# Performance work log

Hardware: AMD Instinct MI355X
Metric: run time of the kernel (lower is better)

The kernel has to match this reference:

```python
import jax, jax.numpy as jnp
import numpy as np

HIDDEN = 1024

def _cat_linear(x, W, b, cat_ids):
    # x: (B,T,Din), W: (C,Din,Dout), b: (C,Dout)
    return jnp.einsum('bti,bio->bto', x, W[cat_ids]) + b[cat_ids][:, None, :]

def _sinusoidal(timesteps, dim):
    # timesteps: (B,T) int -> (B,T,dim)
    t = timesteps.astype(jnp.float32)
    half = dim // 2
    exponent = -jnp.arange(half, dtype=jnp.float32) * (jnp.log(10000.0) / half)
    freqs = t[..., None] * jnp.exp(exponent)
    return jnp.concatenate([jnp.sin(freqs), jnp.cos(freqs)], axis=-1)

def setup_inputs() -> dict:
    key = jax.random.key(0)
    ks = jax.random.split(key, 8)
    B, T, A, H, C = 64, 64, 64, HIDDEN, 16
    actions = jax.random.normal(ks[0], (B, T, A), dtype=jnp.float32)
    timesteps = jax.random.randint(ks[1], (B,), 0, 1000)
    cat_ids = jax.random.randint(ks[2], (B,), 0, C)
    W1 = 0.02 * jax.random.normal(ks[3], (C, A, H), dtype=jnp.float32)
    b1 = jnp.zeros((C, H), dtype=jnp.float32)
    W2 = 0.02 * jax.random.normal(ks[4], (C, 2 * H, H), dtype=jnp.float32)
    b2 = jnp.zeros((C, H), dtype=jnp.float32)
    W3 = 0.02 * jax.random.normal(ks[5], (C, H, H), dtype=jnp.float32)
    b3 = jnp.zeros((C, H), dtype=jnp.float32)
    return {"actions": actions, "timesteps": timesteps, "cat_ids": cat_ids,
            "W1": W1, "b1": b1, "W2": W2, "b2": b2, "W3": W3, "b3": b3}

def reference(actions, timesteps, cat_ids, W1, b1, W2, b2, W3, b3):
    B, T, _ = actions.shape
    ts = jnp.broadcast_to(timesteps[:, None], (B, T))  # (B,T)
    a_emb = _cat_linear(actions, W1, b1, cat_ids)        # (B,T,H)
    tau = _sinusoidal(ts, HIDDEN).astype(a_emb.dtype)    # (B,T,H)
    x = jnp.concatenate([a_emb, tau], axis=-1)           # (B,T,2H)
    h = _cat_linear(x, W2, b2, cat_ids)
    h = h * jax.nn.sigmoid(h)                            # swish
    return _cat_linear(h, W3, b3, cat_ids)               # (B,T,H)
```

## Files before the change

### kernel.cpp

```cpp
#include <hip/hip_runtime.h>
#include <hip/hip_bf16.h>
#include <math.h>


typedef short bf16x8 __attribute__((ext_vector_type(8)));
typedef float floatx4 __attribute__((ext_vector_type(4)));

__device__ inline short f2bf(float f) {
  union { float f; unsigned u; } v; v.f = f;
  unsigned u = v.u;
  return (short)(((u + 0x7fffu + ((u >> 16) & 1u)) >> 16) & 0xffffu);
}

__device__ inline unsigned pk2(float a, float b) {
  union { float f; unsigned u; } x, y; x.f = a; y.f = b;
  unsigned ua = (x.u + 0x7fffu + ((x.u >> 16) & 1u)) >> 16;
  unsigned ub = (y.u + 0x7fffu + ((y.u >> 16) & 1u)) >> 16;
  return (ua & 0xffffu) | (ub << 16);
}

#if __has_builtin(__builtin_amdgcn_global_load_lds)
__device__ inline void async16(float* lds, const float* g) {
  __builtin_amdgcn_global_load_lds(
      (const __attribute__((address_space(1))) unsigned int*)g,
      (__attribute__((address_space(3))) unsigned int*)lds, 16, 0, 0);
}
#define ASYNC_LDS 1
#else
__device__ inline void async16(float* lds, const float* g) {
  *(floatx4*)lds = *(const floatx4*)g;
}
#define ASYNC_LDS 0
#endif

__device__ inline void stage_tile(float* tilebuf, const float* __restrict__ Wsrc,
                                  int tid) {
  const int wave = tid >> 6;
#if ASYNC_LDS
  #pragma unroll
  for (int i = 0; i < 4; ++i) {
    const int s  = i * 256 + tid;
    const int k  = s >> 5;
    const int p  = s & 31;
    const int cc = (p - 4 * (k >> 3)) & 31;
    const float* g = Wsrc + (size_t)k * 1024 + cc * 4;
    float* l = tilebuf + (size_t)(i * 256 + wave * 64) * 4;
    async16(l, g);
  }
#else
  #pragma unroll
  for (int i = 0; i < 4; ++i) {
    const int s  = i * 256 + tid;
    const int k  = s >> 5;
    const int p  = s & 31;
    const int cc = (p - 4 * (k >> 3)) & 31;
    *(floatx4*)(tilebuf + (size_t)s * 4) =
        *(const floatx4*)(Wsrc + (size_t)k * 1024 + cc * 4);
  }
#endif
}

__device__ inline bf16x8 read_bfrag(const float* __restrict__ tile, int col, int quad) {
  const int cc = col >> 2, c3 = col & 3;
  const int p  = (cc + 4 * quad) & 31;
  const float* base = tile + (size_t)p * 4 + c3 + (size_t)(quad * 8) * 128;
  float f[8];
  #pragma unroll
  for (int j = 0; j < 8; ++j) f[j] = base[(size_t)j * 128];
  union { bf16x8 v; unsigned u[4]; } r;
  #pragma unroll
  for (int j = 0; j < 4; ++j) r.u[j] = pk2(f[2 * j], f[2 * j + 1]);
  return r.v;
}

template<int K, bool A_F32, bool SWISH, bool OUT_BF16>
__global__ __launch_bounds__(256) void gemm_kernel(
    const void* __restrict__ Aall, int lda,
    const float* __restrict__ Wall,
    const float* __restrict__ bias,
    const int* __restrict__ cat_ids,
    void* __restrict__ Out, int ldo)
{
  constexpr int N  = 1024;
  constexpr int KT = K / 32;
  __shared__ float wtile[2][32 * 128];
  __shared__ int s_b[80], s_c[80], s_np;

  const int tid = threadIdx.x;
  if (tid < 80) { s_b[tid] = -1; s_c[tid] = 0; }
  __syncthreads();
  if (tid < 64) {
    const int myc = cat_ids[tid];
    int rank = 0, pst = 0, tot = 0;
    #pragma unroll
    for (int c = 0; c < 16; ++c) {
      unsigned long long m = __ballot(myc == c);
      const int cnt = __popcll(m);
      const int pc  = 2 * ((cnt + 1) >> 1);
      if (c < myc)  pst += pc;
      if (c == myc) rank = __popcll(m & ((1ull << tid) - 1ull));
      tot += pc;
    }
    const int slot = pst + rank;
    s_b[slot] = tid;
    s_c[slot] = myc;
    if (tid == 0) s_np = tot >> 1;
  }
  __syncthreads();

  const int e = blockIdx.y;
  if (e >= s_np) return;
  const int b0v = s_b[2 * e];
  int b1 = s_b[2 * e + 1];
  const int c = s_c[2 * e];
  const bool st1 = (b1 >= 0);
  if (!st1) b1 = b0v;

  const int wave = tid >> 6, lane = tid & 63;
  const int quad = lane >> 4, l16 = lane & 15;
  const int wm = wave >> 1, wn = wave & 1;
  const int ns = blockIdx.x * 128;
  const float* Wc = Wall + (size_t)c * K * N + ns;

  const char* arow[4];
  #pragma unroll
  for (int mt = 0; mt < 4; ++mt) {
    const int pr = wm * 64 + mt * 16 + l16;
    const int batch = (pr < 64) ? b0v : b1;
    const int row = batch * 64 + (pr & 63);
    arow[mt] = (const char*)Aall + (size_t)row * lda * (A_F32 ? 4 : 2);
  }

  floatx4 acc[4][4];
  #pragma unroll
  for (int mt = 0; mt < 4; ++mt)
    #pragma unroll
    for (int nt = 0; nt < 4; ++nt)
      acc[mt][nt] = (floatx4){0.f, 0.f, 0.f, 0.f};

  stage_tile(&wtile[0][0], Wc, tid);
  int buf = 0;
  for (int kt = 0; kt < KT; ++kt) {
    __syncthreads();
    if (kt + 1 < KT)
      stage_tile(&wtile[buf ^ 1][0], Wc + (size_t)(kt + 1) * 32 * 1024, tid);

    const float* tp = &wtile[buf][0];
    const int kk = kt * 32 + quad * 8;

    bf16x8 af[4];
    #pragma unroll
    for (int mt = 0; mt < 4; ++mt) {
      if constexpr (A_F32) {
        const floatx4* p = (const floatx4*)(arow[mt] + (size_t)kk * 4);
        floatx4 x0 = p[0], x1 = p[1];
        union { bf16x8 v; unsigned u[4]; } t;
        t.u[0] = pk2(x0[0], x0[1]); t.u[1] = pk2(x0[2], x0[3]);
        t.u[2] = pk2(x1[0], x1[1]); t.u[3] = pk2(x1[2], x1[3]);
        af[mt] = t.v;
      } else {
        af[mt] = *(const bf16x8*)(arow[mt] + (size_t)kk * 2);
      }
    }

    #pragma unroll
    for (int nt = 0; nt < 4; ++nt) {
      bf16x8 bf = read_bfrag(tp, wn * 64 + nt * 16 + l16, quad);
      #pragma unroll
      for (int mt = 0; mt < 4; ++mt)
        acc[mt][nt] = __builtin_amdgcn_mfma_f32_16x16x32_bf16(af[mt], bf, acc[mt][nt], 0, 0, 0);
    }
    buf ^= 1;
  }

  #pragma unroll
  for (int nt = 0; nt < 4; ++nt) {
    const int col = ns + wn * 64 + nt * 16 + l16;
    const float bv = bias[(size_t)c * N + col];
    #pragma unroll
    for (int mt = 0; mt < 4; ++mt) {
      const int prb = wm * 64 + mt * 16 + quad * 4;
      const int batch = (prb < 64) ? b0v : b1;
      const bool do_store = (prb < 64) || st1;
      #pragma unroll
      for (int r = 0; r < 4; ++r) {
        const int row = batch * 64 + ((prb + r) & 63);
        float v = acc[mt][nt][r] + bv;
        if constexpr (SWISH) v = v / (1.f + __expf(-v));
        if (do_store) {
          if constexpr (OUT_BF16)
            ((short*)Out)[(size_t)row * ldo + col] = f2bf(v);
          else
            ((float*)Out)[(size_t)row * ldo + col] = v;
        }
      }
    }
  }
}

__global__ __launch_bounds__(256) void tau_kernel(const int* __restrict__ ts,
                                                  short* __restrict__ x)
{
  const int b = blockIdx.x;
  const float t = (float)ts[b];
  const int tid = threadIdx.x;
  #pragma unroll
  for (int q = 0; q < 4; ++q) {
    const int i  = q * 256 + tid;
    const int hi = i & 511;
    const float e = __expf(-(float)hi * 0.017988946039015980f);
    const float freq = t * e;
    const float v = (i < 512) ? sinf(freq) : cosf(freq);
    const short sv = f2bf(v);
    short* base = x + (size_t)(b * 64) * 2048 + 1024 + i;
    #pragma unroll 4
    for (int tt = 0; tt < 64; ++tt) base[(size_t)tt * 2048] = sv;
  }
}

extern "C" void kernel_launch(void* const* d_in, const int* in_sizes, int n_in,
                              void* d_out, int out_size, void* d_ws, size_t ws_size,
                              hipStream_t stream) {
  const float* actions   = (const float*)d_in[0];
  const int*   timesteps = (const int*)  d_in[1];
  const int*   cat_ids   = (const int*)  d_in[2];
  const float* W1 = (const float*)d_in[3];
  const float* b1 = (const float*)d_in[4];
  const float* W2 = (const float*)d_in[5];
  const float* b2 = (const float*)d_in[6];
  const float* W3 = (const float*)d_in[7];
  const float* b3 = (const float*)d_in[8];

  short* x = (short*)d_ws;
  short* h = x + (size_t)64 * 64 * 2048;

  dim3 grid(8, 40), blk(256);

  gemm_kernel<64, true, false, true><<<grid, blk, 0, stream>>>(
      (const void*)actions, 64, W1, b1, cat_ids, (void*)x, 2048);

  tau_kernel<<<64, 256, 0, stream>>>(timesteps, x);

  gemm_kernel<2048, false, true, true><<<grid, blk, 0, stream>>>(
      (const void*)x, 2048, W2, b2, cat_ids, (void*)h, 1024);

  gemm_kernel<1024, false, false, false><<<grid, blk, 0, stream>>>(
      (const void*)h, 1024, W3, b3, cat_ids, d_out, 1024);
}
```

Before: 374.2 us.

## Restructure GEMM into per-wave triple-buffered pipeline and fuse tau into first GEMM

Each wave now owns a private three-slab LDS buffer for a 32-column weight strip and computes all 128 rows. It prefetches weights two k-steps ahead with async global-to-LDS loads and double-buffers A fragments in registers. Explicit vmcnt waits replace block-wide __syncthreads, removing barrier stalls and letting loads overlap with MFMA work. The code also uses the hardware v_cvt_pk_bf16_f32 instruction for fp32-to-bf16 packing, adds launch_bounds occupancy 2, and folds the sinusoidal tau write into the first GEMM kernel to save a launch. The risks are higher register pressure and that the hand-written waitcnt accounting may be fragile.

After: 432.3 us. 15.5% more time.

```diff
diff --git a/kernel.cpp b/kernel.cpp
--- a/kernel.cpp
+++ b/kernel.cpp
@@ -1,5 +1,4 @@
 #include <hip/hip_runtime.h>
-#include <hip/hip_bf16.h>
 #include <math.h>
 
 
@@ -12,78 +11,113 @@
   return (short)(((u + 0x7fffu + ((u >> 16) & 1u)) >> 16) & 0xffffu);
 }
 
-__device__ inline unsigned pk2(float a, float b) {
-  union { float f; unsigned u; } x, y; x.f = a; y.f = b;
-  unsigned ua = (x.u + 0x7fffu + ((x.u >> 16) & 1u)) >> 16;
-  unsigned ub = (y.u + 0x7fffu + ((y.u >> 16) & 1u)) >> 16;
-  return (ua & 0xffffu) | (ub << 16);
+__device__ __forceinline__ unsigned cvtpk(float a, float b) {
+  unsigned r;
+  asm("v_cvt_pk_bf16_f32 %0, %1, %2" : "=v"(r) : "v"(a), "v"(b));
+  return r;
 }
 
 #if __has_builtin(__builtin_amdgcn_global_load_lds)
-__device__ inline void async16(float* lds, const float* g) {
+#define ASYNC_LDS 1
+__device__ __forceinline__ void async16(const float* g, float* lds) {
   __builtin_amdgcn_global_load_lds(
       (const __attribute__((address_space(1))) unsigned int*)g,
       (__attribute__((address_space(3))) unsigned int*)lds, 16, 0, 0);
 }
-#define ASYNC_LDS 1
 #else
-__device__ inline void async16(float* lds, const float* g) {
+#define ASYNC_LDS 0
+__device__ __forceinline__ void async16(const float* g, float* lds) {
   *(floatx4*)lds = *(const floatx4*)g;
 }
-#define ASYNC_LDS 0
 #endif
 
-__device__ inline void stage_tile(float* tilebuf, const float* __restrict__ Wsrc,
-                                  int tid) {
-  const int wave = tid >> 6;
-#if ASYNC_LDS
-  #pragma unroll
-  for (int i = 0; i < 4; ++i) {
-    const int s  = i * 256 + tid;
-    const int k  = s >> 5;
-    const int p  = s & 31;
-    const int cc = (p - 4 * (k >> 3)) & 31;
-    const float* g = Wsrc + (size_t)k * 1024 + cc * 4;
-    float* l = tilebuf + (size_t)(i * 256 + wave * 64) * 4;
-    async16(l, g);
-  }
-#else
-  #pragma unroll
-  for (int i = 0; i < 4; ++i) {
-    const int s  = i * 256 + tid;
-    const int k  = s >> 5;
-    const int p  = s & 31;
-    const int cc = (p - 4 * (k >> 3)) & 31;
-    *(floatx4*)(tilebuf + (size_t)s * 4) =
-        *(const floatx4*)(Wsrc + (size_t)k * 1024 + cc * 4);
-  }
-#endif
-}
-
-__device__ inline bf16x8 read_bfrag(const float* __restrict__ tile, int col, int quad) {
-  const int cc = col >> 2, c3 = col & 3;
-  const int p  = (cc + 4 * quad) & 31;
-  const float* base = tile + (size_t)p * 4 + c3 + (size_t)(quad * 8) * 128;
-  float f[8];
-  #pragma unroll
-  for (int j = 0; j < 8; ++j) f[j] = base[(size_t)j * 128];
-  union { bf16x8 v; unsigned u[4]; } r;
-  #pragma unroll
-  for (int j = 0; j < 4; ++j) r.u[j] = pk2(f[2 * j], f[2 * j + 1]);
-  return r.v;
-}
-
-template<int K, bool A_F32, bool SWISH, bool OUT_BF16>
-__global__ __launch_bounds__(256) void gemm_kernel(
+__device__ __forceinline__ void gload16(floatx4& d, const void* p) {
+  asm volatile("global_load_dwordx4 %0, %1, off" : "=v"(d) : "v"(p) : "memory");
+}
+template<int N> __device__ __forceinline__ void vm_wait() {
+  asm volatile("s_waitcnt vmcnt(%0)" :: "n"(N) : "memory");
+}
+__device__ __forceinline__ void lgkm0() {
+  asm volatile("s_waitcnt lgkmcnt(0)" ::: "memory");
+}
+
+#define KBODY(VMX, LOADA, DOSTAGE, AIN, AOUT)                                  \
+  {                                                                            \
+    lgkm0();                                                                   \
+    if (LOADA) {                                                               \
+      _Pragma("unroll")                                                        \
+      for (int mt = 0; mt < 8; ++mt) {                                         \
+        const char* p = arow[mt] + aoff;                                       \
+        if constexpr (A_F32) {                                                 \
+          gload16(AOUT[2 * mt], p); gload16(AOUT[2 * mt + 1], p + 16);         \
+        } else {                                                               \
+          gload16(AOUT[mt], p);                                                \
+        }                                                                      \
+      }                                                                        \
+      aoff += 32 * AB;                                                         \
+    }                                                                          \
+    if (DOSTAGE) {                                                             \
+      _Pragma("unroll")                                                        \
+      for (int i = 0; i < 4; ++i)                                              \
+        async16((const float*)(wbp + goff[i]), bs + i * 256);                  \
+      wbp += 32 * 1024 * 4;                                                    \
+    }                                                                          \
+    vm_wait<VMX>();                                                            \
+    __builtin_amdgcn_sched_barrier(0);                                         \
+    bf16x8 af[8];                                                              \
+    _Pragma("unroll")                                                          \
+    for (int mt = 0; mt < 8; ++mt) {                                           \
+      if constexpr (A_F32) {                                                   \
+        union { bf16x8 v; unsigned u[4]; } t;                                  \
+        floatx4 x0 = AIN[2 * mt], x1 = AIN[2 * mt + 1];                        \
+        t.u[0] = cvtpk(x0[0], x0[1]); t.u[1] = cvtpk(x0[2], x0[3]);            \
+        t.u[2] = cvtpk(x1[0], x1[1]); t.u[3] = cvtpk(x1[2], x1[3]);            \
+        af[mt] = t.v;                                                          \
+      } else {                                                                 \
+        union { floatx4 f; bf16x8 v; } t; t.f = AIN[mt]; af[mt] = t.v;         \
+      }                                                                        \
+    }                                                                          \
+    _Pragma("unroll")                                                          \
+    for (int nt = 0; nt < 2; ++nt) {                                           \
+      const float* fp = bc + quad * 256 + ((nt * 16 + l16) ^ (quad << 3));     \
+      float f[8];                                                              \
+      _Pragma("unroll")                                                        \
+      for (int j = 0; j < 8; ++j) f[j] = fp[j * 32];                           \
+      union { bf16x8 v; unsigned u[4]; } bb;                                   \
+      _Pragma("unroll")                                                        \
+      for (int j = 0; j < 4; ++j) bb.u[j] = cvtpk(f[2 * j], f[2 * j + 1]);     \
+      _Pragma("unroll")                                                        \
+      for (int mt = 0; mt < 8; ++mt)                                           \
+        acc[mt][nt] = __builtin_amdgcn_mfma_f32_16x16x32_bf16(                 \
+            af[mt], bb.v, acc[mt][nt], 0, 0, 0);                               \
+    }                                                                          \
+    { float* t_ = bc; bc = bn; bn = bs; bs = t_; }                             \
+  }
+
+template<int K, bool A_F32, bool SWISH, bool OUT_BF16, bool TAU>
+__global__ __launch_bounds__(256, 2) void gemm_kernel(
     const void* __restrict__ Aall, int lda,
     const float* __restrict__ Wall,
     const float* __restrict__ bias,
     const int* __restrict__ cat_ids,
-    void* __restrict__ Out, int ldo)
+    void* __restrict__ Out, int ldo,
+    const int* __restrict__ ts)
 {
-  constexpr int N  = 1024;
+  constexpr int NCOL = 1024;
   constexpr int KT = K / 32;
-  __shared__ float wtile[2][32 * 128];
+  constexpr int AB = A_F32 ? 4 : 2;
+  constexpr int AOPS = A_F32 ? 16 : 8;
+#if ASYNC_LDS
+  constexpr int VM_MAIN = 8 + AOPS;
+  constexpr int VM_T1   = 4 + AOPS;
+#else
+  constexpr int VM_MAIN = AOPS;
+  constexpr int VM_T1   = AOPS;
+#endif
+  static_assert(KT >= 2 && ((KT - 2) % 2 == 0), "K must be a multiple of 64");
+  (void)ts;
+
+  __shared__ float slabs[4][3][1024];
   __shared__ int s_b[80], s_c[80], s_np;
 
   const int tid = threadIdx.x;
@@ -93,12 +127,12 @@
     const int myc = cat_ids[tid];
     int rank = 0, pst = 0, tot = 0;
     #pragma unroll
-    for (int c = 0; c < 16; ++c) {
-      unsigned long long m = __ballot(myc == c);
+    for (int cc = 0; cc < 16; ++cc) {
+      unsigned long long m = __ballot(myc == cc);
       const int cnt = __popcll(m);
       const int pc  = 2 * ((cnt + 1) >> 1);
-      if (c < myc)  pst += pc;
-      if (c == myc) rank = __popcll(m & ((1ull << tid) - 1ull));
+      if (cc < myc)  pst += pc;
+      if (cc == myc) rank = __popcll(m & ((1ull << tid) - 1ull));
       tot += pc;
     }
     const int slot = pst + rank;
@@ -118,68 +152,73 @@
 
   const int wave = tid >> 6, lane = tid & 63;
   const int quad = lane >> 4, l16 = lane & 15;
-  const int wm = wave >> 1, wn = wave & 1;
   const int ns = blockIdx.x * 128;
-  const float* Wc = Wall + (size_t)c * K * N + ns;
-
-  const char* arow[4];
-  #pragma unroll
-  for (int mt = 0; mt < 4; ++mt) {
-    const int pr = wm * 64 + mt * 16 + l16;
+  const int wcol = ns + wave * 32;
+
+  const char* arow[8];
+  #pragma unroll
+  for (int mt = 0; mt < 8; ++mt) {
+    const int pr = mt * 16 + l16;
     const int batch = (pr < 64) ? b0v : b1;
     const int row = batch * 64 + (pr & 63);
-    arow[mt] = (const char*)Aall + (size_t)row * lda * (A_F32 ? 4 : 2);
-  }
-
-  floatx4 acc[4][4];
-  #pragma unroll
-  for (int mt = 0; mt < 4; ++mt)
+    arow[mt] = (const char*)Aall + (size_t)row * lda * AB;
+  }
+
+  int goff[4];
+  #pragma unroll
+  for (int i = 0; i < 4; ++i) {
+    const int s  = i * 64 + lane;
+    const int k  = s >> 3;
+    const int c0 = ((s & 7) << 2) ^ ((s >> 6) << 3);
+    goff[i] = (k * NCOL + c0) * 4;
+  }
+
+  float* const sl0 = &slabs[wave][0][0];
+  float* const sl1 = &slabs[wave][1][0];
+  float* const sl2 = &slabs[wave][2][0];
+  float *bc = sl0, *bn = sl1, *bs = sl2;
+
+  const char* wbp = (const char*)(Wall + (size_t)c * K * NCOL + wcol);
+
+  floatx4 aA[A_F32 ? 16 : 8], aB[A_F32 ? 16 : 8];
+  const int aq = quad * 8 * AB;
+
+  #pragma unroll
+  for (int mt = 0; mt < 8; ++mt) {
+    const char* p = arow[mt] + aq;
+    if constexpr (A_F32) { gload16(aA[2 * mt], p); gload16(aA[2 * mt + 1], p + 16); }
+    else                 { gload16(aA[mt], p); }
+  }
+  #pragma unroll
+  for (int i = 0; i < 4; ++i) async16((const float*)(wbp + goff[i]), sl0 + i * 256);
+  wbp += 32 * NCOL * 4;
+  #pragma unroll
+  for (int i = 0; i < 4; ++i) async16((const float*)(wbp + goff[i]), sl1 + i * 256);
+  wbp += 32 * NCOL * 4;
+
+  int aoff = aq + 32 * AB;
+
+  floatx4 acc[8][2];
+  #pragma unroll
+  for (int mt = 0; mt < 8; ++mt)
     #pragma unroll
-    for (int nt = 0; nt < 4; ++nt)
+    for (int nt = 0; nt < 2; ++nt)
       acc[mt][nt] = (floatx4){0.f, 0.f, 0.f, 0.f};
 
-  stage_tile(&wtile[0][0], Wc, tid);
-  int buf = 0;
-  for (int kt = 0; kt < KT; ++kt) {
-    __syncthreads();
-    if (kt + 1 < KT)
-      stage_tile(&wtile[buf ^ 1][0], Wc + (size_t)(kt + 1) * 32 * 1024, tid);
-
-    const float* tp = &wtile[buf][0];
-    const int kk = kt * 32 + quad * 8;
-
-    bf16x8 af[4];
+  for (int kt = 0; kt + 2 < KT; kt += 2) {
+    KBODY(VM_MAIN, true, true, aA, aB);
+    KBODY(VM_MAIN, true, true, aB, aA);
+  }
+  KBODY(VM_T1, true, false, aA, aB);
+  KBODY(0, false, false, aB, aA);
+
+  #pragma unroll
+  for (int nt = 0; nt < 2; ++nt) {
+    const int col = wcol + nt * 16 + l16;
+    const float bv = bias[(size_t)c * NCOL + col];
     #pragma unroll
-    for (int mt = 0; mt < 4; ++mt) {
-      if constexpr (A_F32) {
-        const floatx4* p = (const floatx4*)(arow[mt] + (size_t)kk * 4);
-        floatx4 x0 = p[0], x1 = p[1];
-        union { bf16x8 v; unsigned u[4]; } t;
-        t.u[0] = pk2(x0[0], x0[1]); t.u[1] = pk2(x0[2], x0[3]);
-        t.u[2] = pk2(x1[0], x1[1]); t.u[3] = pk2(x1[2], x1[3]);
-        af[mt] = t.v;
-      } else {
-        af[mt] = *(const bf16x8*)(arow[mt] + (size_t)kk * 2);
-      }
-    }
-
-    #pragma unroll
-    for (int nt = 0; nt < 4; ++nt) {
-      bf16x8 bf = read_bfrag(tp, wn * 64 + nt * 16 + l16, quad);
-      #pragma unroll
-      for (int mt = 0; mt < 4; ++mt)
-        acc[mt][nt] = __builtin_amdgcn_mfma_f32_16x16x32_bf16(af[mt], bf, acc[mt][nt], 0, 0, 0);
-    }
-    buf ^= 1;
-  }
-
-  #pragma unroll
-  for (int nt = 0; nt < 4; ++nt) {
-    const int col = ns + wn * 64 + nt * 16 + l16;
-    const float bv = bias[(size_t)c * N + col];
-    #pragma unroll
-    for (int mt = 0; mt < 4; ++mt) {
-      const int prb = wm * 64 + mt * 16 + quad * 4;
+    for (int mt = 0; mt < 8; ++mt) {
+      const int prb = mt * 16 + quad * 4;
       const int batch = (prb < 64) ? b0v : b1;
       const bool do_store = (prb < 64) || st1;
       #pragma unroll
@@ -196,25 +235,25 @@
       }
     }
   }
-}
-
-__global__ __launch_bounds__(256) void tau_kernel(const int* __restrict__ ts,
-                                                  short* __restrict__ x)
-{
-  const int b = blockIdx.x;
-  const float t = (float)ts[b];
-  const int tid = threadIdx.x;
-  #pragma unroll
-  for (int q = 0; q < 4; ++q) {
-    const int i  = q * 256 + tid;
-    const int hi = i & 511;
-    const float e = __expf(-(float)hi * 0.017988946039015980f);
-    const float freq = t * e;
-    const float v = (i < 512) ? sinf(freq) : cosf(freq);
-    const short sv = f2bf(v);
-    short* base = x + (size_t)(b * 64) * 2048 + 1024 + i;
+
+  if constexpr (TAU) {
+    const float t0  = (float)ts[b0v];
+    const float t1v = (float)ts[b1];
+    const int ic = ns + (tid & 127);
+    const int hi = ic & 511;
+    const float ef = __expf(-(float)hi * 0.017988946039015980f);
+    float v0, v1;
+    if (ic < 512) { v0 = sinf(t0 * ef); v1 = sinf(t1v * ef); }
+    else          { v0 = cosf(t0 * ef); v1 = cosf(t1v * ef); }
+    const short q0 = f2bf(v0), q1 = f2bf(v1);
+    short* xp = (short*)Out;
+    const int r0 = tid >> 7;
     #pragma unroll 4
-    for (int tt = 0; tt < 64; ++tt) base[(size_t)tt * 2048] = sv;
+    for (int rr = 0; rr < 32; ++rr) {
+      const int rl = r0 + 2 * rr;
+      xp[(size_t)(b0v * 64 + rl) * ldo + 1024 + ic] = q0;
+      if (st1) xp[(size_t)(b1 * 64 + rl) * ldo + 1024 + ic] = q1;
+    }
   }
 }
 
@@ -225,25 +264,21 @@
   const int*   timesteps = (const int*)  d_in[1];
   const int*   cat_ids   = (const int*)  d_in[2];
   const float* W1 = (const float*)d_in[3];
-  const float* b1 = (const float*)d_in[4];
+  const float* B1 = (const float*)d_in[4];
   const float* W2 = (const float*)d_in[5];
-  const float* b2 = (const float*)d_in[6];
+  const float* B2 = (const float*)d_in[6];
   const float* W3 = (const float*)d_in[7];
-  const float* b3 = (const float*)d_in[8];
+  const float* B3 = (const float*)d_in[8];
 
   short* x = (short*)d_ws;
   short* h = x + (size_t)64 * 64 * 2048;
 
   dim3 grid(8, 40), blk(256);
 
-  gemm_kernel<64, true, false, true><<<grid, blk, 0, stream>>>(
-      (const void*)actions, 64, W1, b1, cat_ids, (void*)x, 2048);
-
-  tau_kernel<<<64, 256, 0, stream>>>(timesteps, x);
-
-  gemm_kernel<2048, false, true, true><<<grid, blk, 0, stream>>>(
-      (const void*)x, 2048, W2, b2, cat_ids, (void*)h, 1024);
-
-  gemm_kernel<1024, false, false, false><<<grid, blk, 0, stream>>>(
-      (const void*)h, 1024, W3, b3, cat_ids, d_out, 1024);
-}
+  gemm_kernel<64, true, false, true, true><<<grid, blk, 0, stream>>>(
+      (const void*)actions, 64, W1, B1, cat_ids, (void*)x, 2048, timesteps);
+  gemm_kernel<2048, false, true, true, false><<<grid, blk, 0, stream>>>(
+      (const void*)x, 2048, W2, B2, cat_ids, (void*)h, 1024, nullptr);
+  gemm_kernel<1024, false, false, false, false><<<grid, blk, 0, stream>>>(
+      (const void*)h, 1024, W3, B3, cat_ids, d_out, 1024, nullptr);
+}
```

## Add split-K partitioning with partial-sum reduction for the W2 and W3 GEMMs

Applied to the files above, without the earlier changes.

Adds a z grid dimension that splits the K loop of the second and third grouped GEMMs across several blocks. Each block writes fp32 partial sums to workspace, and a separate reduce kernel adds the bias and applies swish/bf16 conversion. The aim is more parallel blocks on a GPU that the original grid underfills. In exchange it adds extra global memory traffic for the partials and extra kernel launches, and it is enabled only when the workspace is large enough.

After: 364.6 us. -2.6%, faster.

```diff
diff --git a/kernel.cpp b/kernel.cpp
--- a/kernel.cpp
+++ b/kernel.cpp
@@ -5,6 +5,7 @@
 
 typedef short bf16x8 __attribute__((ext_vector_type(8)));
 typedef float floatx4 __attribute__((ext_vector_type(4)));
+typedef unsigned uintx2 __attribute__((ext_vector_type(2)));
 
 __device__ inline short f2bf(float f) {
   union { float f; unsigned u; } v; v.f = f;
@@ -73,7 +74,7 @@
   return r.v;
 }
 
-template<int K, bool A_F32, bool SWISH, bool OUT_BF16>
+template<int K, bool A_F32, bool SWISH, bool OUT_BF16, bool PARTIAL>
 __global__ __launch_bounds__(256) void gemm_kernel(
     const void* __restrict__ Aall, int lda,
     const float* __restrict__ Wall,
@@ -122,6 +123,10 @@
   const int ns = blockIdx.x * 128;
   const float* Wc = Wall + (size_t)c * K * N + ns;
 
+  const int ktc = KT / (int)gridDim.z;
+  const int kt0 = (int)blockIdx.z * ktc;
+  const int kt1 = kt0 + ktc;
+
   const char* arow[4];
   #pragma unroll
   for (int mt = 0; mt < 4; ++mt) {
@@ -138,11 +143,11 @@
     for (int nt = 0; nt < 4; ++nt)
       acc[mt][nt] = (floatx4){0.f, 0.f, 0.f, 0.f};
 
-  stage_tile(&wtile[0][0], Wc, tid);
+  stage_tile(&wtile[0][0], Wc + (size_t)kt0 * 32 * 1024, tid);
   int buf = 0;
-  for (int kt = 0; kt < KT; ++kt) {
+  for (int kt = kt0; kt < kt1; ++kt) {
     __syncthreads();
-    if (kt + 1 < KT)
+    if (kt + 1 < kt1)
       stage_tile(&wtile[buf ^ 1][0], Wc + (size_t)(kt + 1) * 32 * 1024, tid);
 
     const float* tp = &wtile[buf][0];
@@ -173,28 +178,76 @@
     buf ^= 1;
   }
 
-  #pragma unroll
-  for (int nt = 0; nt < 4; ++nt) {
-    const int col = ns + wn * 64 + nt * 16 + l16;
-    const float bv = bias[(size_t)c * N + col];
-    #pragma unroll
-    for (int mt = 0; mt < 4; ++mt) {
-      const int prb = wm * 64 + mt * 16 + quad * 4;
-      const int batch = (prb < 64) ? b0v : b1;
-      const bool do_store = (prb < 64) || st1;
+  if constexpr (PARTIAL) {
+    float* P = (float*)Out + (size_t)blockIdx.z * (4096ull * 1024);
+    #pragma unroll
+    for (int nt = 0; nt < 4; ++nt) {
+      const int col = ns + wn * 64 + nt * 16 + l16;
       #pragma unroll
-      for (int r = 0; r < 4; ++r) {
-        const int row = batch * 64 + ((prb + r) & 63);
-        float v = acc[mt][nt][r] + bv;
-        if constexpr (SWISH) v = v / (1.f + __expf(-v));
-        if (do_store) {
-          if constexpr (OUT_BF16)
-            ((short*)Out)[(size_t)row * ldo + col] = f2bf(v);
-          else
-            ((float*)Out)[(size_t)row * ldo + col] = v;
+      for (int mt = 0; mt < 4; ++mt) {
+        const int prb = wm * 64 + mt * 16 + quad * 4;
+        const int batch = (prb < 64) ? b0v : b1;
+        const bool do_store = (prb < 64) || st1;
+        #pragma unroll
+        for (int r = 0; r < 4; ++r) {
+          const int row = batch * 64 + ((prb + r) & 63);
+          if (do_store) P[(size_t)row * ldo + col] = acc[mt][nt][r];
         }
       }
     }
+  } else {
+    #pragma unroll
+    for (int nt = 0; nt < 4; ++nt) {
+      const int col = ns + wn * 64 + nt * 16 + l16;
+      const float bv = bias[(size_t)c * N + col];
+      #pragma unroll
+      for (int mt = 0; mt < 4; ++mt) {
+        const int prb = wm * 64 + mt * 16 + quad * 4;
+        const int batch = (prb < 64) ? b0v : b1;
+        const bool do_store = (prb < 64) || st1;
+        #pragma unroll
+        for (int r = 0; r < 4; ++r) {
+          const int row = batch * 64 + ((prb + r) & 63);
+          float v = acc[mt][nt][r] + bv;
+          if constexpr (SWISH) v = v / (1.f + __expf(-v));
+          if (do_store) {
+            if constexpr (OUT_BF16)
+              ((short*)Out)[(size_t)row * ldo + col] = f2bf(v);
+            else
+              ((float*)Out)[(size_t)row * ldo + col] = v;
+          }
+        }
+      }
+    }
+  }
+}
+
+template<bool SWISH, bool OUT_BF16>
+__global__ __launch_bounds__(256) void reduce_kernel(
+    const float* __restrict__ P, int nchunk,
+    const float* __restrict__ bias, const int* __restrict__ cat_ids,
+    void* __restrict__ Out, int ldo)
+{
+  const size_t base = ((size_t)blockIdx.x * 256 + threadIdx.x) * 4;
+  const int row = (int)(base >> 10);
+  const int col = (int)(base & 1023);
+  floatx4 s = *(const floatx4*)(P + base);
+  for (int z = 1; z < nchunk; ++z)
+    s += *(const floatx4*)(P + (size_t)z * (4096ull * 1024) + base);
+  const int c = cat_ids[row >> 6];
+  const floatx4 bv = *(const floatx4*)(bias + (size_t)c * 1024 + col);
+  float v[4];
+  #pragma unroll
+  for (int j = 0; j < 4; ++j) {
+    v[j] = s[j] + bv[j];
+    if constexpr (SWISH) v[j] = v[j] / (1.f + __expf(-v[j]));
+  }
+  if constexpr (OUT_BF16) {
+    uintx2 o; o[0] = pk2(v[0], v[1]); o[1] = pk2(v[2], v[3]);
+    *(uintx2*)((short*)Out + (size_t)row * ldo + col) = o;
+  } else {
+    floatx4 o = (floatx4){v[0], v[1], v[2], v[3]};
+    *(floatx4*)((float*)Out + (size_t)row * ldo + col) = o;
   }
 }
 
@@ -225,25 +278,50 @@
   const int*   timesteps = (const int*)  d_in[1];
   const int*   cat_ids   = (const int*)  d_in[2];
   const float* W1 = (const float*)d_in[3];
-  const float* b1 = (const float*)d_in[4];
+  const float* B1 = (const float*)d_in[4];
   const float* W2 = (const float*)d_in[5];
-  const float* b2 = (const float*)d_in[6];
+  const float* B2 = (const float*)d_in[6];
   const float* W3 = (const float*)d_in[7];
-  const float* b3 = (const float*)d_in[8];
+  const float* B3 = (const float*)d_in[8];
 
   short* x = (short*)d_ws;
   short* h = x + (size_t)64 * 64 * 2048;
-
-  dim3 grid(8, 40), blk(256);
-
-  gemm_kernel<64, true, false, true><<<grid, blk, 0, stream>>>(
-      (const void*)actions, 64, W1, b1, cat_ids, (void*)x, 2048);
-
+  float* pbuf = (float*)(h + (size_t)64 * 64 * 1024);
+
+  const size_t CH = 4096ull * 1024 * 4;
+  const size_t used = 24ull * 1024 * 1024;
+  const size_t avail = (ws_size > used) ? (ws_size - used) : 0;
+  int nkz2 = 1, nkz3 = 1;
+  if      (avail >= 8 * CH) { nkz2 = 4; nkz3 = 4; }
+  else if (avail >= 6 * CH) { nkz2 = 4; nkz3 = 2; }
+  else if (avail >= 4 * CH) { nkz2 = 2; nkz3 = 2; }
+  else if (avail >= 2 * CH) { nkz2 = 2; nkz3 = 1; }
+  float* p2 = pbuf;
+  float* p3 = pbuf + (size_t)nkz2 * (CH / 4);
+
+  dim3 blk(256);
+
+  gemm_kernel<64, true, false, true, false><<<dim3(8, 40, 1), blk, 0, stream>>>(
+      (const void*)actions, 64, W1, B1, cat_ids, (void*)x, 2048);
   tau_kernel<<<64, 256, 0, stream>>>(timesteps, x);
 
-  gemm_kernel<2048, false, true, true><<<grid, blk, 0, stream>>>(
-      (const void*)x, 2048, W2, b2, cat_ids, (void*)h, 1024);
-
-  gemm_kernel<1024, false, false, false><<<grid, blk, 0, stream>>>(
-      (const void*)h, 1024, W3, b3, cat_ids, d_out, 1024);
-}
+  if (nkz2 > 1) {
+    gemm_kernel<2048, false, false, false, true><<<dim3(8, 40, nkz2), blk, 0, stream>>>(
+        (const void*)x, 2048, W2, nullptr, cat_ids, (void*)p2, 1024);
+    reduce_kernel<true, true><<<4096, 256, 0, stream>>>(
+        p2, nkz2, B2, cat_ids, (void*)h, 1024);
+  } else {
+    gemm_kernel<2048, false, true, true, false><<<dim3(8, 40, 1), blk, 0, stream>>>(
+        (const void*)x, 2048, W2, B2, cat_ids, (void*)h, 1024);
+  }
+
+  if (nkz3 > 1) {
+    gemm_kernel<1024, false, false, false, true><<<dim3(8, 40, nkz3), blk, 0, stream>>>(
+        (const void*)h, 1024, W3, nullptr, cat_ids, (void*)p3, 1024);
+    reduce_kernel<false, false><<<4096, 256, 0, stream>>>(
+        p3, nkz3, B3, cat_ids, d_out, 1024);
+  } else {
+    gemm_kernel<1024, false, false, false, false><<<dim3(8, 40, 1), blk, 0, stream>>>(
+        (const void*)h, 1024, W3, B3, cat_ids, d_out, 1024);
+  }
+}
```
